# Performance work log

Hardware: AMD Instinct MI355X
Metric: run time of the kernel (lower is better)

The kernel has to match this reference:

```python
import jax, jax.numpy as jnp
import numpy as np

NUM_HEADS = 4
GROUPS = 16
EPS = 1e-5


def setup_inputs() -> dict:
    key = jax.random.key(0)
    ks = jax.random.split(key, 7)
    b, c, hh, ww = 4, 256, 64, 64
    x = jax.random.normal(ks[0], (b, c, hh, ww), dtype=jnp.float32)
    norm_w = 1.0 + 0.1 * jax.random.normal(ks[1], (c,), dtype=jnp.float32)
    norm_b = 0.1 * jax.random.normal(ks[2], (c,), dtype=jnp.float32)
    qkv_w = jax.random.normal(ks[3], (3 * c, c), dtype=jnp.float32) / np.sqrt(c)
    qkv_b = 0.01 * jax.random.normal(ks[4], (3 * c,), dtype=jnp.float32)
    # NOTE: original zero-inits proj_out; we use random weights so the
    # attention path actually affects the output (kernel correctness test).
    proj_w = jax.random.normal(ks[5], (c, c), dtype=jnp.float32) / np.sqrt(c)
    proj_b = jnp.zeros((c,), dtype=jnp.float32)
    return {"x": x, "norm_w": norm_w, "norm_b": norm_b,
            "qkv_w": qkv_w, "qkv_b": qkv_b,
            "proj_w": proj_w, "proj_b": proj_b}


def _group_norm(x, w, b):
    # x: [B, C, T]; GroupNorm32 computes in fp32 (inputs already fp32)
    B, C, T = x.shape
    xg = x.reshape(B, GROUPS, C // GROUPS, T)
    mean = jnp.mean(xg, axis=(2, 3), keepdims=True)
    var = jnp.var(xg, axis=(2, 3), keepdims=True)
    xn = ((xg - mean) * jax.lax.rsqrt(var + EPS)).reshape(B, C, T)
    return xn * w[None, :, None] + b[None, :, None]


def reference(x, norm_w, norm_b, qkv_w, qkv_b, proj_w, proj_b):
    b, c = x.shape[0], x.shape[1]
    spatial = x.shape[2:]
    x2 = x.reshape(b, c, -1)                       # [B, C, T]
    T = x2.shape[-1]
    normed = _group_norm(x2, norm_w, norm_b)
    qkv = jnp.einsum('oc,bct->bot', qkv_w, normed) + qkv_b[None, :, None]
    # faithful reshape: [B, 3C, T] -> [B*H, 3C/H, T], then split in thirds
    qkv = qkv.reshape(b * NUM_HEADS, (3 * c) // NUM_HEADS, T)
    ch = qkv.shape[1] // 3                         # = C / H
    q, k, v = jnp.split(qkv, 3, axis=1)
    scale = 1.0 / np.sqrt(np.sqrt(ch))
    weight = jnp.einsum('bct,bcs->bts', q * scale, k * scale)
    weight = jax.nn.softmax(weight.astype(jnp.float32), axis=-1).astype(qkv.dtype)
    h = jnp.einsum('bts,bcs->bct', weight, v)      # [B*H, ch, T]
    h = h.reshape(b, c, T)
    h = jnp.einsum('oc,bct->bot', proj_w, h) + proj_b[None, :, None]
    return (x2 + h).reshape(b, c, *spatial)
```

## Files before the change

kernel.cpp:

```cpp
#include <hip/hip_runtime.h>

constexpr int kB  = 4;
constexpr int kC  = 256;
constexpr int kT  = 4096;
constexpr int kG  = 16;
constexpr int kCg = kC / kG;
constexpr int kH  = 4;
constexpr int kCh = kC / kH;
constexpr float kEps = 1e-5f;
constexpr float kQScale = 0.125f * 1.4426950408889634f;

typedef short bf16x8 __attribute__((ext_vector_type(8)));
typedef float f32x4  __attribute__((ext_vector_type(4)));
typedef float f32x16 __attribute__((ext_vector_type(16)));

__device__ inline unsigned short f2bf(float f) {
    union { float f; unsigned u; } v; v.f = f;
    unsigned r = v.u + 0x7fffu + ((v.u >> 16) & 1u);
    return (unsigned short)(r >> 16);
}
__device__ inline unsigned pk2bf(float a, float b) {
    return (unsigned)f2bf(a) | ((unsigned)f2bf(b) << 16);
}
__device__ inline unsigned pk2bf_trunc(float a, float b) {
    return __builtin_amdgcn_perm(__float_as_uint(b), __float_as_uint(a), 0x07060302u);
}

__global__ __launch_bounds__(256) void prep_kernel(const float* __restrict__ x,
                                                   float* __restrict__ stats,
                                                   const float* __restrict__ qkv_w,
                                                   const float* __restrict__ proj_w,
                                                   unsigned short* __restrict__ wbf) {
    int tid = threadIdx.x;
    if (blockIdx.x >= 64) {
        int gid = (blockIdx.x - 64) * 256 + tid;
        for (int i = gid; i < 65536; i += 128 * 256) {
            float4 v = (i < 49152) ? ((const float4*)qkv_w)[i]
                                   : ((const float4*)proj_w)[i - 49152];
            *(uint2*)&wbf[(size_t)i * 4] = make_uint2(pk2bf(v.x, v.y), pk2bf(v.z, v.w));
        }
        return;
    }
    int bg = blockIdx.x;
    const float4* xp4 = (const float4*)(x + (size_t)bg * (kCg * kT));
    float s = 0.f, q = 0.f;
    #pragma unroll 4
    for (int i = 0; i < (kCg * kT / 4) / 256; ++i) {
        float4 v = xp4[tid + i * 256];
        s += v.x + v.y + v.z + v.w;
        q += v.x * v.x + v.y * v.y + v.z * v.z + v.w * v.w;
    }
    #pragma unroll
    for (int off = 32; off > 0; off >>= 1) {
        s += __shfl_down(s, off);
        q += __shfl_down(q, off);
    }
    __shared__ float rs[4], rq[4];
    int wid = tid >> 6, lane = tid & 63;
    if (lane == 0) { rs[wid] = s; rq[wid] = q; }
    __syncthreads();
    if (tid == 0) {
        float S = rs[0] + rs[1] + rs[2] + rs[3];
        float Q = rq[0] + rq[1] + rq[2] + rq[3];
        const float invN = 1.0f / (float)(kCg * kT);
        float mean = S * invN;
        float var  = Q * invN - mean * mean;
        stats[bg * 2 + 0] = mean;
        stats[bg * 2 + 1] = rsqrtf(var + kEps);
    }
}

__global__ __launch_bounds__(256) void gn_apply_t_kernel(const float* __restrict__ x,
                                                         const float* __restrict__ stats,
                                                         const float* __restrict__ w,
                                                         const float* __restrict__ bias,
                                                         unsigned short* __restrict__ normT) {
    __shared__ float Ls[64][65];
    int t0 = blockIdx.x * 64;
    int c0 = blockIdx.y * 64;
    int b  = blockIdx.z;
    int tid = threadIdx.x;
    #pragma unroll
    for (int p = 0; p < 4; ++p) {
        int idx = tid + p * 256;
        int cl = idx >> 4, t4 = idx & 15;
        int c = c0 + cl;
        int bg = b * kG + (c >> 4);
        float mean = stats[bg * 2 + 0];
        float rstd = stats[bg * 2 + 1];
        float sw = w[c] * rstd;
        float sb = bias[c] - mean * sw;
        float4 v = *(const float4*)&x[((size_t)b * kC + c) * kT + t0 + t4 * 4];
        Ls[t4 * 4 + 0][cl] = v.x * sw + sb;
        Ls[t4 * 4 + 1][cl] = v.y * sw + sb;
        Ls[t4 * 4 + 2][cl] = v.z * sw + sb;
        Ls[t4 * 4 + 3][cl] = v.w * sw + sb;
    }
    __syncthreads();
    {
        int row = tid >> 2, cq = (tid & 3) * 16;
        unsigned tmp[8];
        #pragma unroll
        for (int i = 0; i < 8; ++i)
            tmp[i] = pk2bf(Ls[row][cq + 2 * i], Ls[row][cq + 2 * i + 1]);
        uint4* dst = (uint4*)&normT[((size_t)b * kT + t0 + row) * kC + c0 + cq];
        dst[0] = make_uint4(tmp[0], tmp[1], tmp[2], tmp[3]);
        dst[1] = make_uint4(tmp[4], tmp[5], tmp[6], tmp[7]);
    }
}

__global__ __launch_bounds__(256) void qkv_gemm_kernel(const unsigned short* __restrict__ wbf,
                                                       const float* __restrict__ qkv_b,
                                                       const unsigned short* __restrict__ normT,
                                                       unsigned short* __restrict__ qTg,
                                                       unsigned short* __restrict__ kTg,
                                                       unsigned short* __restrict__ vCg) {
    constexpr int LDK = 72;
    constexpr int LDV = 136;
    __shared__ __align__(16) unsigned short As[64 * LDK];
    __shared__ __align__(16) unsigned short Bs[128 * LDK];

    int t0 = blockIdx.x * 128;
    int m0 = blockIdx.y * 64;
    int b  = blockIdx.z;
    const unsigned short* Ab = wbf + (size_t)m0 * kC;
    const unsigned short* Bb = normT + (size_t)b * kT * kC;

    int tid = threadIdx.x;
    int wave = tid >> 6, lane = tid & 63;
    int ln15 = lane & 15, quad = lane >> 4;
    int wm = wave >> 1, wt = wave & 1;

    f32x4 acc[2][4] = {};

    for (int k0 = 0; k0 < kC; k0 += 64) {
        __syncthreads();
        #pragma unroll
        for (int p = 0; p < 2; ++p) {
            int idx = tid + p * 256;
            int row = idx >> 3, seg = idx & 7;
            *(uint4*)&As[row * LDK + seg * 8] =
                *(const uint4*)&Ab[(size_t)row * kC + k0 + seg * 8];
        }
        #pragma unroll
        for (int p = 0; p < 4; ++p) {
            int idx = tid + p * 256;
            int row = idx >> 3, seg = idx & 7;
            *(uint4*)&Bs[row * LDK + seg * 8] =
                *(const uint4*)&Bb[(size_t)(t0 + row) * kC + k0 + seg * 8];
        }
        __syncthreads();
        #pragma unroll
        for (int ks = 0; ks < 2; ++ks) {
            bf16x8 af[2], bf[4];
            #pragma unroll
            for (int i = 0; i < 2; ++i)
                af[i] = *(bf16x8*)&As[(wm * 32 + i * 16 + ln15) * LDK + ks * 32 + quad * 8];
            #pragma unroll
            for (int j = 0; j < 4; ++j)
                bf[j] = *(bf16x8*)&Bs[(wt * 64 + j * 16 + ln15) * LDK + ks * 32 + quad * 8];
            #pragma unroll
            for (int i = 0; i < 2; ++i)
                #pragma unroll
                for (int j = 0; j < 4; ++j)
                    acc[i][j] = __builtin_amdgcn_mfma_f32_16x16x32_bf16(
                        af[i], bf[j], acc[i][j], 0, 0, 0);
        }
    }

    int type = (m0 % 192) / 64;
    int h = m0 / 192;
    int bh = b * kH + h;
    __syncthreads();
    #pragma unroll
    for (int i = 0; i < 2; ++i) {
        float4 bv = *(const float4*)&qkv_b[m0 + wm * 32 + i * 16 + quad * 4];
        const float* bp = (const float*)&bv;
        #pragma unroll
        for (int j = 0; j < 4; ++j) {
            int tl = wt * 64 + j * 16 + ln15;
            int c = wm * 32 + i * 16 + quad * 4;
            float v0 = acc[i][j][0] + bp[0];
            float v1 = acc[i][j][1] + bp[1];
            float v2 = acc[i][j][2] + bp[2];
            float v3 = acc[i][j][3] + bp[3];
            if (type == 0) {
                v0 *= kQScale; v1 *= kQScale; v2 *= kQScale; v3 *= kQScale;
            }
            if (type != 2) {
                *(uint2*)&Bs[tl * LDK + c] = make_uint2(pk2bf(v0, v1), pk2bf(v2, v3));
            } else {
                Bs[(c + 0) * LDV + tl] = f2bf(v0);
                Bs[(c + 1) * LDV + tl] = f2bf(v1);
                Bs[(c + 2) * LDV + tl] = f2bf(v2);
                Bs[(c + 3) * LDV + tl] = f2bf(v3);
            }
        }
    }
    __syncthreads();
    if (type != 2) {
        unsigned short* base = ((type == 0) ? qTg : kTg) + (size_t)bh * (kT * kCh);
        #pragma unroll
        for (int p = 0; p < 4; ++p) {
            int f = tid + p * 256;
            int ln = f & 31, hif = (f >> 5) & 1, ks = (f >> 6) & 3, tb = f >> 8;
            *(uint4*)&base[((t0 >> 5) + tb) * 2048 + ks * 512 + hif * 256 + ln * 8] =
                *(uint4*)&Bs[(tb * 32 + ln) * LDK + ks * 16 + hif * 8];
        }
    } else {
        unsigned short* base = vCg + (size_t)bh * (kT * kCh);
        #pragma unroll
        for (int p = 0; p < 4; ++p) {
            int f = tid + p * 256;
            int c = f & 63, hif = (f >> 6) & 1, sg = f >> 7;
            *(uint4*)&base[((t0 >> 4) + sg) * 1024 + hif * 512 + c * 8] =
                *(uint4*)&Bs[c * LDV + sg * 16 + hif * 8];
        }
    }
}

__global__ __launch_bounds__(256, 2) void attn_mfma_kernel(const unsigned short* __restrict__ qTg,
                                                           const unsigned short* __restrict__ kTg,
                                                           const unsigned short* __restrict__ vCg,
                                                           unsigned short* __restrict__ attnT) {
    constexpr int LDPu = 36;
    __shared__ __align__(16) unsigned int Ps[4][32 * LDPu];

    int bh = blockIdx.y;
    int t0 = blockIdx.x * 128;
    int b = bh >> 2, h = bh & 3;

    int tid = threadIdx.x;
    int wave = tid >> 6, lane = tid & 63;
    int ln31 = lane & 31, hi = lane >> 5;
    unsigned int* Pw = &Ps[wave][0];

    const unsigned short* qb = qTg + (size_t)bh * (kT * kCh);
    const unsigned short* kb = kTg + (size_t)bh * (kT * kCh);
    const unsigned short* vb = vCg + (size_t)bh * (kT * kCh);

    bf16x8 qf[4];
    {
        const unsigned short* qp = qb + ((t0 >> 5) + wave) * 2048 + hi * 256 + ln31 * 8;
        #pragma unroll
        for (int ks = 0; ks < 4; ++ks) qf[ks] = *(const bf16x8*)(qp + ks * 512);
    }
    const unsigned short* kptr = kb + hi * 256 + ln31 * 8;
    const unsigned short* vptr = vb + hi * 512 + ln31 * 8;

    bf16x8 kf[8], vf[8];
    #pragma unroll
    for (int i = 0; i < 8; ++i)
        kf[i] = *(const bf16x8*)(kptr + (i >> 2) * 2048 + (i & 3) * 512);
    #pragma unroll
    for (int i = 0; i < 8; ++i)
        vf[i] = *(const bf16x8*)(vptr + (i & 3) * 1024 + (i >> 2) * 256);

    float l_r = 0.f;
    f32x16 accO0 = {}, accO1 = {};
    union PunP { uint4 u; bf16x8 f; };

    for (int s0 = 0; s0 < kT; s0 += 64) {
        f32x16 accS0 = {}, accS1 = {};
        #pragma unroll
        for (int ks = 0; ks < 4; ++ks)
            accS0 = __builtin_amdgcn_mfma_f32_32x32x16_bf16(kf[ks], qf[ks], accS0, 0, 0, 0);
        #pragma unroll
        for (int ks = 0; ks < 4; ++ks)
            accS1 = __builtin_amdgcn_mfma_f32_32x32x16_bf16(kf[4 + ks], qf[ks], accS1, 0, 0, 0);

        if (s0 + 64 < kT) {
            kptr += 4096;
            #pragma unroll
            for (int i = 0; i < 8; ++i)
                kf[i] = *(const bf16x8*)(kptr + (i >> 2) * 2048 + (i & 3) * 512);
        }

        float rs = 0.f;
        #pragma unroll
        for (int g = 0; g < 4; ++g) {
            float p0 = __builtin_amdgcn_exp2f(accS0[4 * g + 0]);
            float p1 = __builtin_amdgcn_exp2f(accS0[4 * g + 1]);
            float p2 = __builtin_amdgcn_exp2f(accS0[4 * g + 2]);
            float p3 = __builtin_amdgcn_exp2f(accS0[4 * g + 3]);
            rs += (p0 + p1) + (p2 + p3);
            int ui = ln31 * LDPu + 4 * g + 2 * hi;
            Pw[ui + 0] = pk2bf_trunc(p0, p1);
            Pw[ui + 1] = pk2bf_trunc(p2, p3);
        }
        #pragma unroll
        for (int g = 0; g < 4; ++g) {
            float p0 = __builtin_amdgcn_exp2f(accS1[4 * g + 0]);
            float p1 = __builtin_amdgcn_exp2f(accS1[4 * g + 1]);
            float p2 = __builtin_amdgcn_exp2f(accS1[4 * g + 2]);
            float p3 = __builtin_amdgcn_exp2f(accS1[4 * g + 3]);
            rs += (p0 + p1) + (p2 + p3);
            int ui = ln31 * LDPu + 16 + 4 * g + 2 * hi;
            Pw[ui + 0] = pk2bf_trunc(p0, p1);
            Pw[ui + 1] = pk2bf_trunc(p2, p3);
        }
        rs += __shfl_xor(rs, 32);
        l_r += rs;
        __asm__ __volatile__("" ::: "memory");

        #pragma unroll
        for (int i = 0; i < 4; ++i) {
            PunP pk;
            pk.u = *(const uint4*)&Pw[ln31 * LDPu + i * 8 + hi * 4];
            accO0 = __builtin_amdgcn_mfma_f32_32x32x16_bf16(vf[i],     pk.f, accO0, 0, 0, 0);
            accO1 = __builtin_amdgcn_mfma_f32_32x32x16_bf16(vf[4 + i], pk.f, accO1, 0, 0, 0);
        }

        if (s0 + 64 < kT) {
            vptr += 4096;
            #pragma unroll
            for (int i = 0; i < 8; ++i)
                vf[i] = *(const bf16x8*)(vptr + (i & 3) * 1024 + (i >> 2) * 256);
        }
        __asm__ __volatile__("" ::: "memory");
    }

    float linv = 1.0f / l_r;
    int t = t0 + wave * 32 + ln31;
    #pragma unroll
    for (int ct = 0; ct < 2; ++ct) {
        const f32x16& ao = ct ? accO1 : accO0;
        #pragma unroll
        for (int g = 0; g < 4; ++g) {
            int c = h * kCh + ct * 32 + 8 * g + 4 * hi;
            float v0 = ao[4 * g + 0] * linv;
            float v1 = ao[4 * g + 1] * linv;
            float v2 = ao[4 * g + 2] * linv;
            float v3 = ao[4 * g + 3] * linv;
            *(uint2*)&attnT[((size_t)b * kT + t) * kC + c] =
                make_uint2(pk2bf(v0, v1), pk2bf(v2, v3));
        }
    }
}

__global__ __launch_bounds__(256) void proj_gemm_kernel(const unsigned short* __restrict__ wpbf,
                                                        const float* __restrict__ proj_b,
                                                        const unsigned short* __restrict__ attnT,
                                                        const float* __restrict__ x,
                                                        float* __restrict__ out) {
    constexpr int LDK = 72;
    __shared__ __align__(16) unsigned short As[64 * LDK];
    __shared__ __align__(16) unsigned short Bs[128 * LDK];

    int t0 = blockIdx.x * 128;
    int m0 = blockIdx.y * 64;
    int b  = blockIdx.z;
    const unsigned short* Ab = wpbf + (size_t)m0 * kC;
    const unsigned short* Bb = attnT + (size_t)b * kT * kC;

    int tid = threadIdx.x;
    int wave = tid >> 6, lane = tid & 63;
    int ln15 = lane & 15, quad = lane >> 4;
    int wm = wave >> 1, wt = wave & 1;

    f32x4 acc[2][4] = {};

    for (int k0 = 0; k0 < kC; k0 += 64) {
        __syncthreads();
        #pragma unroll
        for (int p = 0; p < 2; ++p) {
            int idx = tid + p * 256;
            int row = idx >> 3, seg = idx & 7;
            *(uint4*)&As[row * LDK + seg * 8] =
                *(const uint4*)&Ab[(size_t)row * kC + k0 + seg * 8];
        }
        #pragma unroll
        for (int p = 0; p < 4; ++p) {
            int idx = tid + p * 256;
            int row = idx >> 3, seg = idx & 7;
            *(uint4*)&Bs[row * LDK + seg * 8] =
                *(const uint4*)&Bb[(size_t)(t0 + row) * kC + k0 + seg * 8];
        }
        __syncthreads();
        #pragma unroll
        for (int ks = 0; ks < 2; ++ks) {
            bf16x8 af[2], bf[4];
            #pragma unroll
            for (int i = 0; i < 2; ++i)
                af[i] = *(bf16x8*)&As[(wm * 32 + i * 16 + ln15) * LDK + ks * 32 + quad * 8];
            #pragma unroll
            for (int j = 0; j < 4; ++j)
                bf[j] = *(bf16x8*)&Bs[(wt * 64 + j * 16 + ln15) * LDK + ks * 32 + quad * 8];
            #pragma unroll
            for (int i = 0; i < 2; ++i)
                #pragma unroll
                for (int j = 0; j < 4; ++j)
                    acc[i][j] = __builtin_amdgcn_mfma_f32_16x16x32_bf16(
                        af[i], bf[j], acc[i][j], 0, 0, 0);
        }
    }

    #pragma unroll
    for (int i = 0; i < 2; ++i) {
        float4 bv = *(const float4*)&proj_b[m0 + wm * 32 + i * 16 + quad * 4];
        const float* bp = (const float*)&bv;
        #pragma unroll
        for (int j = 0; j < 4; ++j) {
            int t = t0 + wt * 64 + j * 16 + ln15;
            int mbase = m0 + wm * 32 + i * 16 + quad * 4;
            #pragma unroll
            for (int r = 0; r < 4; ++r) {
                size_t off = ((size_t)b * kC + mbase + r) * kT + t;
                out[off] = acc[i][j][r] + bp[r] + x[off];
            }
        }
    }
}

extern "C" void kernel_launch(void* const* d_in, const int* in_sizes, int n_in,
                              void* d_out, int out_size, void* d_ws, size_t ws_size,
                              hipStream_t stream) {
    const float* x      = (const float*)d_in[0];
    const float* norm_w = (const float*)d_in[1];
    const float* norm_b = (const float*)d_in[2];
    const float* qkv_w  = (const float*)d_in[3];
    const float* qkv_b  = (const float*)d_in[4];
    const float* proj_w = (const float*)d_in[5];
    const float* proj_b = (const float*)d_in[6];
    float* out = (float*)d_out;

    float* stats = (float*)d_ws;
    unsigned short* wsbf  = (unsigned short*)((float*)d_ws + 128);
    unsigned short* normT = wsbf;
    unsigned short* wbf   = normT + (size_t)kB * kT * kC;
    unsigned short* qTp   = wbf + 262144;
    unsigned short* kTp   = qTp + (size_t)kB * kH * kT * kCh;
    unsigned short* vCp   = kTp + (size_t)kB * kH * kT * kCh;
    unsigned short* attnT = vCp + (size_t)kB * kH * kT * kCh;
    unsigned short* wpbf  = wbf + 196608;

    prep_kernel<<<192, 256, 0, stream>>>(x, stats, qkv_w, proj_w, wbf);
    gn_apply_t_kernel<<<dim3(kT / 64, kC / 64, kB), 256, 0, stream>>>(
        x, stats, norm_w, norm_b, normT);
    qkv_gemm_kernel<<<dim3(kT / 128, 12, kB), 256, 0, stream>>>(
        wbf, qkv_b, normT, qTp, kTp, vCp);
    attn_mfma_kernel<<<dim3(kT / 128, kB * kH), 256, 0, stream>>>(qTp, kTp, vCp, attnT);
    proj_gemm_kernel<<<dim3(kT / 128, kC / 64, kB), 256, 0, stream>>>(
        wpbf, proj_b, attnT, x, out);
}
```

Before: 212.9 us.

## Split attention KV range across wave pairs and pass P via permlane swap

The attention kernel now handles 64 query rows per block, with waves split into two query tiles and two halves of the key sequence. Partial outputs and row sums are combined through shared memory at the end. The P tile is rearranged in registers with v_permlane32_swap instead of being written to and read back from LDS, and the loop processes 32 keys per step with smaller register footprints so occupancy can rise to 4 blocks. This costs a final cross-wave reduction and loses the software prefetch of K/V, so load latency is now exposed within each iteration.

```diff
diff --git a/kernel.cpp b/kernel.cpp
--- a/kernel.cpp
+++ b/kernel.cpp
@@ -24,6 +24,9 @@
 }
 __device__ inline unsigned pk2bf_trunc(float a, float b) {
     return __builtin_amdgcn_perm(__float_as_uint(b), __float_as_uint(a), 0x07060302u);
+}
+__device__ inline void pls32(unsigned& a, unsigned& b) {
+    __asm__("v_permlane32_swap_b32 %0, %1" : "+v"(a), "+v"(b));
 }
 
 __global__ __launch_bounds__(256) void prep_kernel(const float* __restrict__ x,
@@ -219,21 +222,22 @@
     }
 }
 
-__global__ __launch_bounds__(256, 2) void attn_mfma_kernel(const unsigned short* __restrict__ qTg,
+__global__ __launch_bounds__(256, 4) void attn_mfma_kernel(const unsigned short* __restrict__ qTg,
                                                            const unsigned short* __restrict__ kTg,
                                                            const unsigned short* __restrict__ vCg,
                                                            unsigned short* __restrict__ attnT) {
-    constexpr int LDPu = 36;
-    __shared__ __align__(16) unsigned int Ps[4][32 * LDPu];
+    __shared__ float Ored[2][32][64];
+    __shared__ float Lred[2][64];
 
     int bh = blockIdx.y;
-    int t0 = blockIdx.x * 128;
+    int t0 = blockIdx.x * 64;
     int b = bh >> 2, h = bh & 3;
 
     int tid = threadIdx.x;
     int wave = tid >> 6, lane = tid & 63;
     int ln31 = lane & 31, hi = lane >> 5;
-    unsigned int* Pw = &Ps[wave][0];
+    int tc = wave & 1;
+    int sh = wave >> 1;
 
     const unsigned short* qb = qTg + (size_t)bh * (kT * kCh);
     const unsigned short* kb = kTg + (size_t)bh * (kT * kCh);
@@ -241,99 +245,117 @@
 
     bf16x8 qf[4];
     {
-        const unsigned short* qp = qb + ((t0 >> 5) + wave) * 2048 + hi * 256 + ln31 * 8;
+        const unsigned short* qp = qb + ((size_t)(t0 >> 5) + tc) * 2048 + hi * 256 + ln31 * 8;
         #pragma unroll
         for (int ks = 0; ks < 4; ++ks) qf[ks] = *(const bf16x8*)(qp + ks * 512);
     }
-    const unsigned short* kptr = kb + hi * 256 + ln31 * 8;
-    const unsigned short* vptr = vb + hi * 512 + ln31 * 8;
-
-    bf16x8 kf[8], vf[8];
-    #pragma unroll
-    for (int i = 0; i < 8; ++i)
-        kf[i] = *(const bf16x8*)(kptr + (i >> 2) * 2048 + (i & 3) * 512);
-    #pragma unroll
-    for (int i = 0; i < 8; ++i)
-        vf[i] = *(const bf16x8*)(vptr + (i & 3) * 1024 + (i >> 2) * 256);
+
+    const unsigned short* kp = kb + (size_t)sh * 131072 + hi * 256 + ln31 * 8;
+    const unsigned short* vp = vb + (size_t)sh * 131072 + hi * 512 + ln31 * 8;
 
     float l_r = 0.f;
     f32x16 accO0 = {}, accO1 = {};
     union PunP { uint4 u; bf16x8 f; };
 
-    for (int s0 = 0; s0 < kT; s0 += 64) {
-        f32x16 accS0 = {}, accS1 = {};
-        #pragma unroll
-        for (int ks = 0; ks < 4; ++ks)
-            accS0 = __builtin_amdgcn_mfma_f32_32x32x16_bf16(kf[ks], qf[ks], accS0, 0, 0, 0);
-        #pragma unroll
-        for (int ks = 0; ks < 4; ++ks)
-            accS1 = __builtin_amdgcn_mfma_f32_32x32x16_bf16(kf[4 + ks], qf[ks], accS1, 0, 0, 0);
-
-        if (s0 + 64 < kT) {
-            kptr += 4096;
-            #pragma unroll
-            for (int i = 0; i < 8; ++i)
-                kf[i] = *(const bf16x8*)(kptr + (i >> 2) * 2048 + (i & 3) * 512);
-        }
-
-        float rs = 0.f;
-        #pragma unroll
-        for (int g = 0; g < 4; ++g) {
-            float p0 = __builtin_amdgcn_exp2f(accS0[4 * g + 0]);
-            float p1 = __builtin_amdgcn_exp2f(accS0[4 * g + 1]);
-            float p2 = __builtin_amdgcn_exp2f(accS0[4 * g + 2]);
-            float p3 = __builtin_amdgcn_exp2f(accS0[4 * g + 3]);
-            rs += (p0 + p1) + (p2 + p3);
-            int ui = ln31 * LDPu + 4 * g + 2 * hi;
-            Pw[ui + 0] = pk2bf_trunc(p0, p1);
-            Pw[ui + 1] = pk2bf_trunc(p2, p3);
-        }
-        #pragma unroll
-        for (int g = 0; g < 4; ++g) {
-            float p0 = __builtin_amdgcn_exp2f(accS1[4 * g + 0]);
-            float p1 = __builtin_amdgcn_exp2f(accS1[4 * g + 1]);
-            float p2 = __builtin_amdgcn_exp2f(accS1[4 * g + 2]);
-            float p3 = __builtin_amdgcn_exp2f(accS1[4 * g + 3]);
-            rs += (p0 + p1) + (p2 + p3);
-            int ui = ln31 * LDPu + 16 + 4 * g + 2 * hi;
-            Pw[ui + 0] = pk2bf_trunc(p0, p1);
-            Pw[ui + 1] = pk2bf_trunc(p2, p3);
-        }
-        rs += __shfl_xor(rs, 32);
-        l_r += rs;
-        __asm__ __volatile__("" ::: "memory");
-
-        #pragma unroll
-        for (int i = 0; i < 4; ++i) {
-            PunP pk;
-            pk.u = *(const uint4*)&Pw[ln31 * LDPu + i * 8 + hi * 4];
-            accO0 = __builtin_amdgcn_mfma_f32_32x32x16_bf16(vf[i],     pk.f, accO0, 0, 0, 0);
-            accO1 = __builtin_amdgcn_mfma_f32_32x32x16_bf16(vf[4 + i], pk.f, accO1, 0, 0, 0);
-        }
-
-        if (s0 + 64 < kT) {
-            vptr += 4096;
-            #pragma unroll
-            for (int i = 0; i < 8; ++i)
-                vf[i] = *(const bf16x8*)(vptr + (i & 3) * 1024 + (i >> 2) * 256);
-        }
-        __asm__ __volatile__("" ::: "memory");
-    }
-
-    float linv = 1.0f / l_r;
-    int t = t0 + wave * 32 + ln31;
-    #pragma unroll
-    for (int ct = 0; ct < 2; ++ct) {
-        const f32x16& ao = ct ? accO1 : accO0;
-        #pragma unroll
-        for (int g = 0; g < 4; ++g) {
-            int c = h * kCh + ct * 32 + 8 * g + 4 * hi;
-            float v0 = ao[4 * g + 0] * linv;
-            float v1 = ao[4 * g + 1] * linv;
-            float v2 = ao[4 * g + 2] * linv;
-            float v3 = ao[4 * g + 3] * linv;
-            *(uint2*)&attnT[((size_t)b * kT + t) * kC + c] =
-                make_uint2(pk2bf(v0, v1), pk2bf(v2, v3));
+    #pragma unroll 1
+    for (int it = 0; it < 64; ++it) {
+        bf16x8 kf0 = *(const bf16x8*)(kp);
+        bf16x8 kf1 = *(const bf16x8*)(kp + 512);
+        bf16x8 kf2 = *(const bf16x8*)(kp + 1024);
+        bf16x8 kf3 = *(const bf16x8*)(kp + 1536);
+        bf16x8 vf00 = *(const bf16x8*)(vp);
+        bf16x8 vf10 = *(const bf16x8*)(vp + 256);
+        bf16x8 vf01 = *(const bf16x8*)(vp + 1024);
+        bf16x8 vf11 = *(const bf16x8*)(vp + 1024 + 256);
+        kp += 2048; vp += 2048;
+
+        f32x16 accS = {};
+        accS = __builtin_amdgcn_mfma_f32_32x32x16_bf16(kf0, qf[0], accS, 0, 0, 0);
+        accS = __builtin_amdgcn_mfma_f32_32x32x16_bf16(kf1, qf[1], accS, 0, 0, 0);
+        accS = __builtin_amdgcn_mfma_f32_32x32x16_bf16(kf2, qf[2], accS, 0, 0, 0);
+        accS = __builtin_amdgcn_mfma_f32_32x32x16_bf16(kf3, qf[3], accS, 0, 0, 0);
+
+        unsigned u00, u01, u10, u11, u20, u21, u30, u31;
+        {
+            float p0 = __builtin_amdgcn_exp2f(accS[0]);
+            float p1 = __builtin_amdgcn_exp2f(accS[1]);
+            float p2 = __builtin_amdgcn_exp2f(accS[2]);
+            float p3 = __builtin_amdgcn_exp2f(accS[3]);
+            l_r += (p0 + p1) + (p2 + p3);
+            u00 = pk2bf_trunc(p0, p1); u01 = pk2bf_trunc(p2, p3);
+        }
+        {
+            float p0 = __builtin_amdgcn_exp2f(accS[4]);
+            float p1 = __builtin_amdgcn_exp2f(accS[5]);
+            float p2 = __builtin_amdgcn_exp2f(accS[6]);
+            float p3 = __builtin_amdgcn_exp2f(accS[7]);
+            l_r += (p0 + p1) + (p2 + p3);
+            u10 = pk2bf_trunc(p0, p1); u11 = pk2bf_trunc(p2, p3);
+        }
+        {
+            float p0 = __builtin_amdgcn_exp2f(accS[8]);
+            float p1 = __builtin_amdgcn_exp2f(accS[9]);
+            float p2 = __builtin_amdgcn_exp2f(accS[10]);
+            float p3 = __builtin_amdgcn_exp2f(accS[11]);
+            l_r += (p0 + p1) + (p2 + p3);
+            u20 = pk2bf_trunc(p0, p1); u21 = pk2bf_trunc(p2, p3);
+        }
+        {
+            float p0 = __builtin_amdgcn_exp2f(accS[12]);
+            float p1 = __builtin_amdgcn_exp2f(accS[13]);
+            float p2 = __builtin_amdgcn_exp2f(accS[14]);
+            float p3 = __builtin_amdgcn_exp2f(accS[15]);
+            l_r += (p0 + p1) + (p2 + p3);
+            u30 = pk2bf_trunc(p0, p1); u31 = pk2bf_trunc(p2, p3);
+        }
+
+        pls32(u00, u10);
+        pls32(u01, u11);
+        pls32(u20, u30);
+        pls32(u21, u31);
+        PunP F0, F1;
+        F0.u = make_uint4(u00, u01, u10, u11);
+        F1.u = make_uint4(u20, u21, u30, u31);
+
+        accO0 = __builtin_amdgcn_mfma_f32_32x32x16_bf16(vf00, F0.f, accO0, 0, 0, 0);
+        accO1 = __builtin_amdgcn_mfma_f32_32x32x16_bf16(vf10, F0.f, accO1, 0, 0, 0);
+        accO0 = __builtin_amdgcn_mfma_f32_32x32x16_bf16(vf01, F1.f, accO0, 0, 0, 0);
+        accO1 = __builtin_amdgcn_mfma_f32_32x32x16_bf16(vf11, F1.f, accO1, 0, 0, 0);
+    }
+
+    l_r += __shfl_xor(l_r, 32);
+
+    if (sh == 1) {
+        #pragma unroll
+        for (int e = 0; e < 16; ++e) {
+            Ored[tc][e][lane]      = accO0[e];
+            Ored[tc][16 + e][lane] = accO1[e];
+        }
+        Lred[tc][lane] = l_r;
+    }
+    __syncthreads();
+    if (sh == 0) {
+        #pragma unroll
+        for (int e = 0; e < 16; ++e) {
+            accO0[e] += Ored[tc][e][lane];
+            accO1[e] += Ored[tc][16 + e][lane];
+        }
+        l_r += Lred[tc][lane];
+        float linv = 1.0f / l_r;
+        int t = t0 + tc * 32 + ln31;
+        #pragma unroll
+        for (int ct = 0; ct < 2; ++ct) {
+            const f32x16& ao = ct ? accO1 : accO0;
+            #pragma unroll
+            for (int g = 0; g < 4; ++g) {
+                int c = h * kCh + ct * 32 + 8 * g + 4 * hi;
+                float v0 = ao[4 * g + 0] * linv;
+                float v1 = ao[4 * g + 1] * linv;
+                float v2 = ao[4 * g + 2] * linv;
+                float v3 = ao[4 * g + 3] * linv;
+                *(uint2*)&attnT[((size_t)b * kT + t) * kC + c] =
+                    make_uint2(pk2bf(v0, v1), pk2bf(v2, v3));
+            }
         }
     }
 }
@@ -439,7 +461,7 @@
         x, stats, norm_w, norm_b, normT);
     qkv_gemm_kernel<<<dim3(kT / 128, 12, kB), 256, 0, stream>>>(
         wbf, qkv_b, normT, qTp, kTp, vCp);
-    attn_mfma_kernel<<<dim3(kT / 128, kB * kH), 256, 0, stream>>>(qTp, kTp, vCp, attnT);
+    attn_mfma_kernel<<<dim3(kT / 64, kB * kH), 256, 0, stream>>>(qTp, kTp, vCp, attnT);
     proj_gemm_kernel<<<dim3(kT / 128, kC / 64, kB), 256, 0, stream>>>(
         wpbf, proj_b, attnT, x, out);
 }
```

Measured after the change: 212.6 us. About the same (-0.1%).
